# Kernel optimization log

Hardware: AMD Instinct MI355X
Metric: run time of the kernel (lower is better)

The kernel has to match this reference:

```python
import jax, jax.numpy as jnp
import numpy as np

N = 50000
IN_DIM = 256
HID = 64
HEADS = 4
OUT_DIM = 40
E = 800000
NEG_SLOPE = 0.2


def setup_inputs() -> dict:
    key = jax.random.key(0)
    ks = jax.random.split(key, 12)
    x = jax.random.normal(ks[0], (N, IN_DIM), dtype=jnp.float32)
    edge_index = jax.random.randint(ks[1], (2, E), 0, N, dtype=jnp.int64)
    s = 0.05
    W1 = jax.random.normal(ks[2], (IN_DIM, HEADS * HID), dtype=jnp.float32) * s
    att_src1 = jax.random.normal(ks[3], (HEADS, HID), dtype=jnp.float32) * s
    att_dst1 = jax.random.normal(ks[4], (HEADS, HID), dtype=jnp.float32) * s
    b1 = jnp.zeros((HEADS * HID,), dtype=jnp.float32)
    W2 = jax.random.normal(ks[5], (HEADS * HID, OUT_DIM), dtype=jnp.float32) * s
    att_src2 = jax.random.normal(ks[6], (1, OUT_DIM), dtype=jnp.float32) * s
    att_dst2 = jax.random.normal(ks[7], (1, OUT_DIM), dtype=jnp.float32) * s
    b2 = jnp.zeros((OUT_DIM,), dtype=jnp.float32)
    return {"x": x, "edge_index": edge_index, "W1": W1, "att_src1": att_src1,
            "att_dst1": att_dst1, "b1": b1, "W2": W2, "att_src2": att_src2,
            "att_dst2": att_dst2, "b2": b2}


def _gat_conv(x, src, dst, W, a_src, a_dst, b, heads, out_ch, concat):
    n = x.shape[0]
    h = (x @ W).reshape(n, heads, out_ch)              # [N,H,C]
    alpha_s = jnp.einsum('nhc,hc->nh', h, a_src)       # [N,H]
    alpha_d = jnp.einsum('nhc,hc->nh', h, a_dst)
    e = jax.nn.leaky_relu(alpha_s[src] + alpha_d[dst], NEG_SLOPE)  # [E,H]
    # segment softmax over destination neighborhoods
    m = jax.ops.segment_max(e, dst, num_segments=n)    # [N,H]
    ex = jnp.exp(e - m[dst])
    denom = jax.ops.segment_sum(ex, dst, num_segments=n)
    alpha = ex / (denom[dst] + 1e-16)                  # [E,H]
    out = jax.ops.segment_sum(h[src] * alpha[:, :, None], dst, num_segments=n)  # [N,H,C]
    out = out.reshape(n, heads * out_ch) if concat else out.mean(axis=1)
    return out + b


def reference(x, edge_index, W1, att_src1, att_dst1, b1, W2, att_src2, att_dst2, b2):
    # PyG GATConv adds self-loops by default
    loops = jnp.arange(N, dtype=edge_index.dtype)
    src = jnp.concatenate([edge_index[0], loops])
    dst = jnp.concatenate([edge_index[1], loops])
    h = _gat_conv(x, src, dst, W1, att_src1, att_dst1, b1, HEADS, HID, True)
    h = jax.nn.elu(h)
    h = _gat_conv(h, src, dst, W2, att_src2, att_dst2, b2, 1, OUT_DIM, False)
    return jax.nn.log_softmax(h, axis=1)
```

## Files before the change

### kernel.cpp

```cpp
#include <hip/hip_runtime.h>
#include <hip/hip_bf16.h>
#include <math.h>

#define NNODES 50000
#define M_PAD  50048
#define IN_DIM 256
#define HID 64
#define HEADS 4
#define OUT_DIM 40
#define NEDGES 800000
#define ETOT (NEDGES + NNODES)
#define NEG_SLOPE 0.2f
#define MAXDEG 64

typedef __attribute__((ext_vector_type(8))) short bf16x8;
typedef __attribute__((ext_vector_type(4))) float f32x4;
typedef __attribute__((ext_vector_type(2))) float f32x2;

__device__ __forceinline__ ushort f2bf(float f) {
    uint u = __float_as_uint(f);
    u += 0x7FFF + ((u >> 16) & 1);
    return (ushort)(u >> 16);
}
__device__ __forceinline__ uint fkey(float f) {
    uint u = __float_as_uint(f);
    return (u & 0x80000000u) ? ~u : (u | 0x80000000u);
}
__device__ __forceinline__ float fdec(uint k) {
    return (k & 0x80000000u) ? __uint_as_float(k & 0x7fffffffu) : __uint_as_float(~k);
}
__device__ __forceinline__ float wave_reduce_max(float v) {
    #pragma unroll
    for (int off = 32; off > 0; off >>= 1) v = fmaxf(v, __shfl_xor(v, off));
    return v;
}
__device__ __forceinline__ float wave_reduce_sum(float v) {
    #pragma unroll
    for (int off = 32; off > 0; off >>= 1) v += __shfl_xor(v, off);
    return v;
}

__device__ __forceinline__ void accum8p(f32x2* acc2, uint4 hv, float wgt) {
    f32x2 wv = {wgt, wgt};
    f32x2 v;
    v.x = __uint_as_float(hv.x << 16); v.y = __uint_as_float(hv.x & 0xFFFF0000u);
    acc2[0] += v * wv;
    v.x = __uint_as_float(hv.y << 16); v.y = __uint_as_float(hv.y & 0xFFFF0000u);
    acc2[1] += v * wv;
    v.x = __uint_as_float(hv.z << 16); v.y = __uint_as_float(hv.z & 0xFFFF0000u);
    acc2[2] += v * wv;
    v.x = __uint_as_float(hv.w << 16); v.y = __uint_as_float(hv.w & 0xFFFF0000u);
    acc2[3] += v * wv;
}
__device__ __forceinline__ float lrw(float e, float mm) {
    return __expf(fmaxf(e, NEG_SLOPE * e) - mm);
}

__global__ __launch_bounds__(256) void cvt_weights_kernel(const float* __restrict__ W1,
                                                          const float* __restrict__ W2,
                                                          ushort* __restrict__ W1t,
                                                          ushort* __restrict__ W2tb) {
    int b = blockIdx.x, t = threadIdx.x;
    if (b < 256) {
        W1t[b * 256 + t] = f2bf(W1[t * 256 + b]);
    } else {
        int idx = (b - 256) * 256 + t;
        if (idx < 48 * 264) {
            int n = idx / 264, k = idx % 264;
            W2tb[idx] = (n < OUT_DIM && k < 256) ? f2bf(W2[k * OUT_DIM + n]) : (ushort)0;
        }
    }
}

__global__ void scatter_kernel(const int* __restrict__ ei,
                               int* __restrict__ counts, int* __restrict__ col) {
    int idx = blockIdx.x * blockDim.x + threadIdx.x;
    if (idx >= ETOT) return;
    int s, d;
    if (idx < NEDGES) { s = ei[idx]; d = ei[NEDGES + idx]; }
    else { s = idx - NEDGES; d = s; }
    int pos = atomicAdd(&counts[d], 1);
    if (pos < MAXDEG) col[d * MAXDEG + pos] = s;
}

__global__ __launch_bounds__(256) void gemm1_fused(const float* __restrict__ x,
                                                   const ushort* __restrict__ W1t,
                                                   const float* __restrict__ asrc,
                                                   const float* __restrict__ adst,
                                                   ushort* __restrict__ h1b,
                                                   float* __restrict__ as1,
                                                   float* __restrict__ ad1,
                                                   uint* __restrict__ gb) {
    __shared__ ushort As[64 * 32];
    __shared__ ushort Bs[256 * 32];
    __shared__ uint smax[4];
    int t = threadIdx.x;
    int l = t & 63, wn = t >> 6;
    int m0 = blockIdx.x * 64;
    int lrow = l & 15, lks = l >> 4;
    int ks = lks ^ ((lrow >> 1) & 3);

    f32x4 acc[4][4];
    #pragma unroll
    for (int i = 0; i < 4; i++)
        #pragma unroll
        for (int j = 0; j < 4; j++) acc[i][j] = (f32x4){0.f, 0.f, 0.f, 0.f};

    for (int k0 = 0; k0 < 256; k0 += 32) {
        #pragma unroll
        for (int i = 0; i < 2; i++) {
            int idx = t + 256 * i;
            int row = idx >> 3, c4 = idx & 7;
            int grow = m0 + row;
            float4 v = make_float4(0.f, 0.f, 0.f, 0.f);
            if (grow < NNODES) v = *reinterpret_cast<const float4*>(x + (size_t)grow * 256 + k0 + c4 * 4);
            uint2 p;
            p.x = (uint)f2bf(v.x) | ((uint)f2bf(v.y) << 16);
            p.y = (uint)f2bf(v.z) | ((uint)f2bf(v.w) << 16);
            int slot = (c4 >> 1) ^ ((row >> 1) & 3);
            *reinterpret_cast<uint2*>(&As[row * 32 + slot * 8 + (c4 & 1) * 4]) = p;
        }
        #pragma unroll
        for (int i = 0; i < 4; i++) {
            int idx = t + 256 * i;
            int row = idx >> 2, skb = idx & 3;
            uint4 bv = *reinterpret_cast<const uint4*>(W1t + (size_t)row * 256 + k0 + skb * 8);
            int slot = skb ^ ((row >> 1) & 3);
            *reinterpret_cast<uint4*>(&Bs[row * 32 + slot * 8]) = bv;
        }
        __syncthreads();
        bf16x8 a_frag[4], b_frag[4];
        #pragma unroll
        for (int mf = 0; mf < 4; mf++)
            a_frag[mf] = *reinterpret_cast<const bf16x8*>(&As[(mf * 16 + lrow) * 32 + ks * 8]);
        #pragma unroll
        for (int nf = 0; nf < 4; nf++)
            b_frag[nf] = *reinterpret_cast<const bf16x8*>(&Bs[(wn * 64 + nf * 16 + lrow) * 32 + ks * 8]);
        #pragma unroll
        for (int mf = 0; mf < 4; mf++)
            #pragma unroll
            for (int nf = 0; nf < 4; nf++)
                acc[mf][nf] = __builtin_amdgcn_mfma_f32_16x16x32_bf16(a_frag[mf], b_frag[nf], acc[mf][nf], 0, 0, 0);
        __syncthreads();
    }

    #pragma unroll
    for (int mf = 0; mf < 4; mf++)
        #pragma unroll
        for (int nf = 0; nf < 4; nf++) {
            int col = wn * 64 + nf * 16 + lrow;
            #pragma unroll
            for (int r = 0; r < 4; r++) {
                int row = m0 + mf * 16 + lks * 4 + r;
                h1b[(size_t)row * 256 + col] = f2bf(acc[mf][nf][r]);
            }
        }

    float a_s[4], a_d[4];
    #pragma unroll
    for (int nf = 0; nf < 4; nf++) {
        a_s[nf] = asrc[wn * 64 + nf * 16 + lrow];
        a_d[nf] = adst[wn * 64 + nf * 16 + lrow];
    }
    float ps[4][4], pd[4][4];
    #pragma unroll
    for (int mf = 0; mf < 4; mf++)
        #pragma unroll
        for (int r = 0; r < 4; r++) {
            float s = 0.f, d = 0.f;
            #pragma unroll
            for (int nf = 0; nf < 4; nf++) {
                s += acc[mf][nf][r] * a_s[nf];
                d += acc[mf][nf][r] * a_d[nf];
            }
            ps[mf][r] = s; pd[mf][r] = d;
        }
    #pragma unroll
    for (int off = 1; off < 16; off <<= 1)
        #pragma unroll
        for (int mf = 0; mf < 4; mf++)
            #pragma unroll
            for (int r = 0; r < 4; r++) {
                ps[mf][r] += __shfl_xor(ps[mf][r], off);
                pd[mf][r] += __shfl_xor(pd[mf][r], off);
            }
    if (lrow == 0) {
        #pragma unroll
        for (int mf = 0; mf < 4; mf++)
            #pragma unroll
            for (int r = 0; r < 4; r++) {
                int row = m0 + mf * 16 + lks * 4 + r;
                if (row < NNODES) {
                    as1[row * 4 + wn] = ps[mf][r];
                    ad1[row * 4 + wn] = pd[mf][r];
                }
            }
    }
    float vmax = -INFINITY;
    #pragma unroll
    for (int mf = 0; mf < 4; mf++)
        #pragma unroll
        for (int r = 0; r < 4; r++) {
            int row = m0 + mf * 16 + lks * 4 + r;
            if (row < NNODES) vmax = fmaxf(vmax, ps[mf][r]);
        }
    vmax = fmaxf(vmax, __shfl_xor(vmax, 16));
    vmax = fmaxf(vmax, __shfl_xor(vmax, 32));
    if (l == 0) smax[wn] = fkey(vmax);
    __syncthreads();
    if (t < 4) atomicMax(&gb[t], smax[t]);
}

__device__ __forceinline__ void agg1_chunk(const int* __restrict__ p, int base, int deg,
                                           const float* __restrict__ as1,
                                           const ushort* __restrict__ h1b,
                                           int myh, uint jo, float adn, float mm,
                                           f32x2* acc2, float& ls) {
    int4 ca = *reinterpret_cast<const int4*>(p);
    int4 cb = *reinterpret_cast<const int4*>(p + 4);
    int s0 = (base + 0 < deg) ? ca.x : 0;
    int s1 = (base + 1 < deg) ? ca.y : 0;
    int s2 = (base + 2 < deg) ? ca.z : 0;
    int s3 = (base + 3 < deg) ? ca.w : 0;
    int s4 = (base + 4 < deg) ? cb.x : 0;
    int s5 = (base + 5 < deg) ? cb.y : 0;
    int s6 = (base + 6 < deg) ? cb.z : 0;
    int s7 = (base + 7 < deg) ? cb.w : 0;
    float q0 = as1[(uint)(s0 * 4 + myh)];
    float q1 = as1[(uint)(s1 * 4 + myh)];
    float q2 = as1[(uint)(s2 * 4 + myh)];
    float q3 = as1[(uint)(s3 * 4 + myh)];
    float q4 = as1[(uint)(s4 * 4 + myh)];
    float q5 = as1[(uint)(s5 * 4 + myh)];
    float q6 = as1[(uint)(s6 * 4 + myh)];
    float q7 = as1[(uint)(s7 * 4 + myh)];
    uint4 h0 = *reinterpret_cast<const uint4*>(h1b + (((uint)s0 << 8) + jo));
    uint4 h1v = *reinterpret_cast<const uint4*>(h1b + (((uint)s1 << 8) + jo));
    uint4 h2v = *reinterpret_cast<const uint4*>(h1b + (((uint)s2 << 8) + jo));
    uint4 h3v = *reinterpret_cast<const uint4*>(h1b + (((uint)s3 << 8) + jo));
    uint4 h4v = *reinterpret_cast<const uint4*>(h1b + (((uint)s4 << 8) + jo));
    uint4 h5v = *reinterpret_cast<const uint4*>(h1b + (((uint)s5 << 8) + jo));
    uint4 h6v = *reinterpret_cast<const uint4*>(h1b + (((uint)s6 << 8) + jo));
    uint4 h7v = *reinterpret_cast<const uint4*>(h1b + (((uint)s7 << 8) + jo));
    float w0 = (base + 0 < deg) ? lrw(q0 + adn, mm) : 0.f;
    float w1 = (base + 1 < deg) ? lrw(q1 + adn, mm) : 0.f;
    float w2 = (base + 2 < deg) ? lrw(q2 + adn, mm) : 0.f;
    float w3 = (base + 3 < deg) ? lrw(q3 + adn, mm) : 0.f;
    float w4 = (base + 4 < deg) ? lrw(q4 + adn, mm) : 0.f;
    float w5 = (base + 5 < deg) ? lrw(q5 + adn, mm) : 0.f;
    float w6 = (base + 6 < deg) ? lrw(q6 + adn, mm) : 0.f;
    float w7 = (base + 7 < deg) ? lrw(q7 + adn, mm) : 0.f;
    ls += ((w0 + w1) + (w2 + w3)) + ((w4 + w5) + (w6 + w7));
    accum8p(acc2, h0, w0); accum8p(acc2, h1v, w1);
    accum8p(acc2, h2v, w2); accum8p(acc2, h3v, w3);
    accum8p(acc2, h4v, w4); accum8p(acc2, h5v, w5);
    accum8p(acc2, h6v, w6); accum8p(acc2, h7v, w7);
}

__global__ __launch_bounds__(256) void agg1_kernel(const ushort* __restrict__ h1b,
                                                   const float* __restrict__ as1,
                                                   const float* __restrict__ ad1,
                                                   const int* __restrict__ cnt,
                                                   const int* __restrict__ col,
                                                   const float* __restrict__ b1,
                                                   const uint* __restrict__ gb,
                                                   ushort* __restrict__ out1b) {
    int tid = threadIdx.x;
    int lane = tid & 63, wid = tid >> 6;
    int n = blockIdx.x * 4 + wid;
    int j = lane & 31, half = lane >> 5;
    int myh = j >> 3;
    int deg = min(cnt[n], MAXDEG);
    const int* cp = col + n * MAXDEG;

    float adn = ad1[n * 4 + myh];
    float g = fdec(gb[myh]);
    float mt = g + adn;
    float mm = fmaxf(mt, NEG_SLOPE * mt);

    f32x2 acc2[4];
    #pragma unroll
    for (int k = 0; k < 4; k++) acc2[k] = (f32x2){0.f, 0.f};
    float ls = 0.f;
    uint jo = (uint)(j * 8);

    for (int done = 0; done < deg; done += 16) {
        int base = done + half * 8;
        agg1_chunk(cp + base, base, deg, as1, h1b, myh, jo, adn, mm, acc2, ls);
    }
    #pragma unroll
    for (int k = 0; k < 4; k++) {
        acc2[k].x += __shfl_xor(acc2[k].x, 32);
        acc2[k].y += __shfl_xor(acc2[k].y, 32);
    }
    ls += __shfl_xor(ls, 32);

    if (lane < 32) {
        float dinv = 1.f / (ls + 1e-16f);
        float4 bA = *reinterpret_cast<const float4*>(b1 + j * 8);
        float4 bB = *reinterpret_cast<const float4*>(b1 + j * 8 + 4);
        float o[8];
        o[0] = acc2[0].x * dinv + bA.x; o[1] = acc2[0].y * dinv + bA.y;
        o[2] = acc2[1].x * dinv + bA.z; o[3] = acc2[1].y * dinv + bA.w;
        o[4] = acc2[2].x * dinv + bB.x; o[5] = acc2[2].y * dinv + bB.y;
        o[6] = acc2[3].x * dinv + bB.z; o[7] = acc2[3].y * dinv + bB.w;
        uint4 pk;
        #pragma unroll
        for (int e8 = 0; e8 < 8; e8++) o[e8] = o[e8] > 0.f ? o[e8] : expm1f(o[e8]);
        pk.x = (uint)f2bf(o[0]) | ((uint)f2bf(o[1]) << 16);
        pk.y = (uint)f2bf(o[2]) | ((uint)f2bf(o[3]) << 16);
        pk.z = (uint)f2bf(o[4]) | ((uint)f2bf(o[5]) << 16);
        pk.w = (uint)f2bf(o[6]) | ((uint)f2bf(o[7]) << 16);
        *reinterpret_cast<uint4*>(out1b + ((uint)n * 256 + jo)) = pk;
    }
}

__global__ __launch_bounds__(256) void gemm2_fused(const ushort* __restrict__ Ag,
                                                   const ushort* __restrict__ Bg,
                                                   const float* __restrict__ a2s,
                                                   const float* __restrict__ a2d,
                                                   ushort* __restrict__ h2b,
                                                   float* __restrict__ as2,
                                                   float* __restrict__ ad2,
                                                   uint* __restrict__ gb) {
    __shared__ ushort Bs[48 * 264];
    __shared__ uint smax;
    int t = threadIdx.x;
    int l = t & 63, w = t >> 6;
    int lrow = l & 15, lks = l >> 4;
    if (t == 0) smax = 0u;
    for (int idx = t; idx < 48 * 264 / 8; idx += 256)
        reinterpret_cast<uint4*>(Bs)[idx] = reinterpret_cast<const uint4*>(Bg)[idx];
    __syncthreads();

    int m0 = blockIdx.x * 64 + w * 16;
    f32x4 acc[3];
    #pragma unroll
    for (int nf = 0; nf < 3; nf++) acc[nf] = (f32x4){0.f, 0.f, 0.f, 0.f};

    #pragma unroll
    for (int k0 = 0; k0 < 256; k0 += 32) {
        bf16x8 af = *reinterpret_cast<const bf16x8*>(Ag + (size_t)(m0 + lrow) * 256 + k0 + lks * 8);
        #pragma unroll
        for (int nf = 0; nf < 3; nf++) {
            bf16x8 bf = *reinterpret_cast<const bf16x8*>(&Bs[(nf * 16 + lrow) * 264 + k0 + lks * 8]);
            acc[nf] = __builtin_amdgcn_mfma_f32_16x16x32_bf16(af, bf, acc[nf], 0, 0, 0);
        }
    }

    float a_s[3], a_d[3];
    #pragma unroll
    for (int nf = 0; nf < 3; nf++) {
        int c = nf * 16 + lrow;
        a_s[nf] = (c < OUT_DIM) ? a2s[c] : 0.f;
        a_d[nf] = (c < OUT_DIM) ? a2d[c] : 0.f;
    }
    float ps[4], pd[4];
    #pragma unroll
    for (int r = 0; r < 4; r++) {
        float s = 0.f, d = 0.f;
        #pragma unroll
        for (int nf = 0; nf < 3; nf++) { s += acc[nf][r] * a_s[nf]; d += acc[nf][r] * a_d[nf]; }
        ps[r] = s; pd[r] = d;
    }
    #pragma unroll
    for (int nf = 0; nf < 3; nf++) {
        int c = nf * 16 + lrow;
        if (c < OUT_DIM) {
            #pragma unroll
            for (int r = 0; r < 4; r++) {
                int row = m0 + lks * 4 + r;
                if (row < NNODES) h2b[(size_t)row * OUT_DIM + c] = f2bf(acc[nf][r]);
            }
        }
    }
    #pragma unroll
    for (int off = 1; off < 16; off <<= 1)
        #pragma unroll
        for (int r = 0; r < 4; r++) {
            ps[r] += __shfl_xor(ps[r], off);
            pd[r] += __shfl_xor(pd[r], off);
        }
    if (lrow == 0) {
        #pragma unroll
        for (int r = 0; r < 4; r++) {
            int row = m0 + lks * 4 + r;
            if (row < NNODES) { as2[row] = ps[r]; ad2[row] = pd[r]; }
        }
    }
    float vmax = -INFINITY;
    #pragma unroll
    for (int r = 0; r < 4; r++) {
        int row = m0 + lks * 4 + r;
        if (row < NNODES) vmax = fmaxf(vmax, ps[r]);
    }
    vmax = fmaxf(vmax, __shfl_xor(vmax, 16));
    vmax = fmaxf(vmax, __shfl_xor(vmax, 32));
    if (l == 0) atomicMax(&smax, fkey(vmax));
    __syncthreads();
    if (t == 0) atomicMax(&gb[4], smax);
}

__device__ __forceinline__ void agg2_chunk(const int* __restrict__ p, int base, int deg,
                                           const float* __restrict__ as2,
                                           const ushort* __restrict__ h2b,
                                           bool act, uint jo, float adn, float mm,
                                           f32x2& a2, float& ls) {
    int4 ca = *reinterpret_cast<const int4*>(p);
    int4 cb = *reinterpret_cast<const int4*>(p + 4);
    int s0 = (base + 0 < deg) ? ca.x : 0;
    int s1 = (base + 1 < deg) ? ca.y : 0;
    int s2 = (base + 2 < deg) ? ca.z : 0;
    int s3 = (base + 3 < deg) ? ca.w : 0;
    int s4 = (base + 4 < deg) ? cb.x : 0;
    int s5 = (base + 5 < deg) ? cb.y : 0;
    int s6 = (base + 6 < deg) ? cb.z : 0;
    int s7 = (base + 7 < deg) ? cb.w : 0;
    float q0 = as2[(uint)s0], q1 = as2[(uint)s1], q2 = as2[(uint)s2], q3 = as2[(uint)s3];
    float q4 = as2[(uint)s4], q5 = as2[(uint)s5], q6 = as2[(uint)s6], q7 = as2[(uint)s7];
    uint v0 = 0, v1 = 0, v2 = 0, v3 = 0, v4 = 0, v5 = 0, v6 = 0, v7 = 0;
    if (act) {
        v0 = *reinterpret_cast<const uint*>(h2b + ((uint)s0 * 40 + jo));
        v1 = *reinterpret_cast<const uint*>(h2b + ((uint)s1 * 40 + jo));
        v2 = *reinterpret_cast<const uint*>(h2b + ((uint)s2 * 40 + jo));
        v3 = *reinterpret_cast<const uint*>(h2b + ((uint)s3 * 40 + jo));
        v4 = *reinterpret_cast<const uint*>(h2b + ((uint)s4 * 40 + jo));
        v5 = *reinterpret_cast<const uint*>(h2b + ((uint)s5 * 40 + jo));
        v6 = *reinterpret_cast<const uint*>(h2b + ((uint)s6 * 40 + jo));
        v7 = *reinterpret_cast<const uint*>(h2b + ((uint)s7 * 40 + jo));
    }
    float w0 = (base + 0 < deg) ? lrw(q0 + adn, mm) : 0.f;
    float w1 = (base + 1 < deg) ? lrw(q1 + adn, mm) : 0.f;
    float w2 = (base + 2 < deg) ? lrw(q2 + adn, mm) : 0.f;
    float w3 = (base + 3 < deg) ? lrw(q3 + adn, mm) : 0.f;
    float w4 = (base + 4 < deg) ? lrw(q4 + adn, mm) : 0.f;
    float w5 = (base + 5 < deg) ? lrw(q5 + adn, mm) : 0.f;
    float w6 = (base + 6 < deg) ? lrw(q6 + adn, mm) : 0.f;
    float w7 = (base + 7 < deg) ? lrw(q7 + adn, mm) : 0.f;
    ls += ((w0 + w1) + (w2 + w3)) + ((w4 + w5) + (w6 + w7));
    f32x2 hv;
    hv.x = __uint_as_float(v0 << 16); hv.y = __uint_as_float(v0 & 0xFFFF0000u);
    a2 += hv * (f32x2){w0, w0};
    hv.x = __uint_as_float(v1 << 16); hv.y = __uint_as_float(v1 & 0xFFFF0000u);
    a2 += hv * (f32x2){w1, w1};
    hv.x = __uint_as_float(v2 << 16); hv.y = __uint_as_float(v2 & 0xFFFF0000u);
    a2 += hv * (f32x2){w2, w2};
    hv.x = __uint_as_float(v3 << 16); hv.y = __uint_as_float(v3 & 0xFFFF0000u);
    a2 += hv * (f32x2){w3, w3};
    hv.x = __uint_as_float(v4 << 16); hv.y = __uint_as_float(v4 & 0xFFFF0000u);
    a2 += hv * (f32x2){w4, w4};
    hv.x = __uint_as_float(v5 << 16); hv.y = __uint_as_float(v5 & 0xFFFF0000u);
    a2 += hv * (f32x2){w5, w5};
    hv.x = __uint_as_float(v6 << 16); hv.y = __uint_as_float(v6 & 0xFFFF0000u);
    a2 += hv * (f32x2){w6, w6};
    hv.x = __uint_as_float(v7 << 16); hv.y = __uint_as_float(v7 & 0xFFFF0000u);
    a2 += hv * (f32x2){w7, w7};
}

__global__ __launch_bounds__(256) void agg2_kernel(const ushort* __restrict__ h2b,
                                                   const float* __restrict__ as2,
                                                   const float* __restrict__ ad2,
                                                   const int* __restrict__ cnt,
                                                   const int* __restrict__ col,
                                                   const float* __restrict__ b2,
                                                   const uint* __restrict__ gb,
                                                   float* __restrict__ out) {
    int tid = threadIdx.x;
    int lane = tid & 63, wid = tid >> 6;
    int n = blockIdx.x * 4 + wid;
    int j = lane & 31, half = lane >> 5;
    int deg = min(cnt[n], MAXDEG);
    const int* cp = col + n * MAXDEG;
    float adn = ad2[n];
    float g = fdec(gb[4]);
    float mt = g + adn;
    float mm = fmaxf(mt, NEG_SLOPE * mt);

    bool act = j < 20;
    uint jo = (uint)(j * 2);
    f32x2 a2 = {0.f, 0.f};
    float ls = 0.f;

    for (int done = 0; done < deg; done += 16) {
        int base = done + half * 8;
        agg2_chunk(cp + base, base, deg, as2, h2b, act, jo, adn, mm, a2, ls);
    }
    a2.x += __shfl_xor(a2.x, 32);
    a2.y += __shfl_xor(a2.y, 32);
    ls += __shfl_xor(ls, 32);

    bool lead = lane < 20;
    float v0 = -INFINITY, v1 = -INFINITY;
    if (lead) {
        float2 bb = *reinterpret_cast<const float2*>(b2 + 2 * j);
        float dinv = 1.f / (ls + 1e-16f);
        v0 = a2.x * dinv + bb.x;
        v1 = a2.y * dinv + bb.y;
    }
    float mx = wave_reduce_max(fmaxf(v0, v1));
    float es = lead ? (__expf(v0 - mx) + __expf(v1 - mx)) : 0.f;
    float ssum = wave_reduce_sum(es);
    float lg = logf(ssum);
    if (lead) {
        float2 o2 = make_float2(v0 - mx - lg, v1 - mx - lg);
        *reinterpret_cast<float2*>(out + (size_t)n * OUT_DIM + 2 * j) = o2;
    }
}

extern "C" void kernel_launch(void* const* d_in, const int* in_sizes, int n_in,
                              void* d_out, int out_size, void* d_ws, size_t ws_size,
                              hipStream_t stream) {
    const float* x        = (const float*)d_in[0];
    const int*   ei       = (const int*)d_in[1];
    const float* W1       = (const float*)d_in[2];
    const float* att_src1 = (const float*)d_in[3];
    const float* att_dst1 = (const float*)d_in[4];
    const float* b1       = (const float*)d_in[5];
    const float* W2       = (const float*)d_in[6];
    const float* att_src2 = (const float*)d_in[7];
    const float* att_dst2 = (const float*)d_in[8];
    const float* b2       = (const float*)d_in[9];
    float* out = (float*)d_out;

    char* ws = (char*)d_ws;
    auto alloc = [&](size_t bytes) {
        char* p = ws;
        ws += (bytes + 255) & ~(size_t)255;
        return p;
    };
    ushort* h1b    = (ushort*)alloc((size_t)M_PAD * 256 * 2);
    ushort* out1b  = (ushort*)alloc((size_t)M_PAD * 256 * 2);
    ushort* W1t    = (ushort*)alloc((size_t)256 * 256 * 2);
    ushort* W2tb   = (ushort*)alloc((size_t)48 * 264 * 2);
    ushort* h2b    = (ushort*)alloc((size_t)NNODES * OUT_DIM * 2);
    float*  as1    = (float*)alloc((size_t)NNODES * 4 * 4);
    float*  ad1    = (float*)alloc((size_t)NNODES * 4 * 4);
    float*  as2    = (float*)alloc((size_t)NNODES * 4);
    float*  ad2    = (float*)alloc((size_t)NNODES * 4);
    int*    counts = (int*)alloc((size_t)(NNODES + 8) * 4);
    uint*   gmaxb  = (uint*)(counts + NNODES);
    int*    col    = (int*)alloc((size_t)NNODES * MAXDEG * 4);
    if ((size_t)(ws - (char*)d_ws) > ws_size) return;

    hipMemsetAsync(counts, 0, (size_t)(NNODES + 8) * 4, stream);

    cvt_weights_kernel<<<256 + (48 * 264 + 255) / 256, 256, 0, stream>>>(W1, W2, W1t, W2tb);

    int eb = (ETOT + 255) / 256;
    scatter_kernel<<<eb, 256, 0, stream>>>(ei, counts, col);

    gemm1_fused<<<M_PAD / 64, 256, 0, stream>>>(x, W1t, att_src1, att_dst1,
                                                h1b, as1, ad1, gmaxb);
    agg1_kernel<<<NNODES / 4, 256, 0, stream>>>(h1b, as1, ad1, counts, col, b1, gmaxb, out1b);

    gemm2_fused<<<M_PAD / 64, 256, 0, stream>>>(out1b, W2tb, att_src2, att_dst2,
                                                h2b, as2, ad2, gmaxb);
    agg2_kernel<<<NNODES / 4, 256, 0, stream>>>(h2b, as2, ad2, counts, col, b2, gmaxb, out);
}
```

Measured before the change: 213.3 us.

## Fold layer-2 attention projections into agg1 and merge prep kernels

```diff
diff --git a/kernel.cpp b/kernel.cpp
--- a/kernel.cpp
+++ b/kernel.cpp
@@ -39,7 +39,6 @@
     for (int off = 32; off > 0; off >>= 1) v += __shfl_xor(v, off);
     return v;
 }
-
 __device__ __forceinline__ void accum8p(f32x2* acc2, uint4 hv, float wgt) {
     f32x2 wv = {wgt, wgt};
     f32x2 v;
@@ -56,31 +55,41 @@
     return __expf(fmaxf(e, NEG_SLOPE * e) - mm);
 }
 
-__global__ __launch_bounds__(256) void cvt_weights_kernel(const float* __restrict__ W1,
-                                                          const float* __restrict__ W2,
-                                                          ushort* __restrict__ W1t,
-                                                          ushort* __restrict__ W2tb) {
+__global__ void prep_kernel(const float* __restrict__ W1, const float* __restrict__ W2,
+                            const float* __restrict__ a2s, const float* __restrict__ a2d,
+                            const int* __restrict__ ei,
+                            ushort* __restrict__ W1t, ushort* __restrict__ W2tb,
+                            float* __restrict__ wa_s, float* __restrict__ wa_d,
+                            int* __restrict__ counts, int* __restrict__ col) {
     int b = blockIdx.x, t = threadIdx.x;
     if (b < 256) {
         W1t[b * 256 + t] = f2bf(W1[t * 256 + b]);
-    } else {
+    } else if (b < 306) {
         int idx = (b - 256) * 256 + t;
         if (idx < 48 * 264) {
             int n = idx / 264, k = idx % 264;
             W2tb[idx] = (n < OUT_DIM && k < 256) ? f2bf(W2[k * OUT_DIM + n]) : (ushort)0;
         }
-    }
-}
-
-__global__ void scatter_kernel(const int* __restrict__ ei,
-                               int* __restrict__ counts, int* __restrict__ col) {
-    int idx = blockIdx.x * blockDim.x + threadIdx.x;
-    if (idx >= ETOT) return;
-    int s, d;
-    if (idx < NEDGES) { s = ei[idx]; d = ei[NEDGES + idx]; }
-    else { s = idx - NEDGES; d = s; }
-    int pos = atomicAdd(&counts[d], 1);
-    if (pos < MAXDEG) col[d * MAXDEG + pos] = s;
+    } else if (b == 306) {
+        float ss = 0.f, sd = 0.f;
+        #pragma unroll 8
+        for (int c = 0; c < OUT_DIM; c++) {
+            float wv = W2[t * OUT_DIM + c];
+            ss += wv * a2s[c];
+            sd += wv * a2d[c];
+        }
+        wa_s[t] = ss;
+        wa_d[t] = sd;
+    } else {
+        int idx = (b - 307) * 256 + t;
+        if (idx < ETOT) {
+            int s, d;
+            if (idx < NEDGES) { s = ei[idx]; d = ei[NEDGES + idx]; }
+            else { s = idx - NEDGES; d = s; }
+            int pos = atomicAdd(&counts[d], 1);
+            if (pos < MAXDEG) col[d * MAXDEG + pos] = s;
+        }
+    }
 }
 
 __global__ __launch_bounds__(256) void gemm1_fused(const float* __restrict__ x,
@@ -264,7 +273,11 @@
                                                    const int* __restrict__ col,
                                                    const float* __restrict__ b1,
                                                    const uint* __restrict__ gb,
-                                                   ushort* __restrict__ out1b) {
+                                                   const float* __restrict__ wa_s,
+                                                   const float* __restrict__ wa_d,
+                                                   ushort* __restrict__ out1b,
+                                                   float* __restrict__ as2,
+                                                   float* __restrict__ ad2) {
     int tid = threadIdx.x;
     int lane = tid & 63, wid = tid >> 6;
     int n = blockIdx.x * 4 + wid;
@@ -295,18 +308,32 @@
     }
     ls += __shfl_xor(ls, 32);
 
+    float dinv = 1.f / (ls + 1e-16f);
+    float4 bA = *reinterpret_cast<const float4*>(b1 + j * 8);
+    float4 bB = *reinterpret_cast<const float4*>(b1 + j * 8 + 4);
+    float4 wsA = *reinterpret_cast<const float4*>(wa_s + j * 8);
+    float4 wsB = *reinterpret_cast<const float4*>(wa_s + j * 8 + 4);
+    float4 wdA = *reinterpret_cast<const float4*>(wa_d + j * 8);
+    float4 wdB = *reinterpret_cast<const float4*>(wa_d + j * 8 + 4);
+    float o[8];
+    o[0] = acc2[0].x * dinv + bA.x; o[1] = acc2[0].y * dinv + bA.y;
+    o[2] = acc2[1].x * dinv + bA.z; o[3] = acc2[1].y * dinv + bA.w;
+    o[4] = acc2[2].x * dinv + bB.x; o[5] = acc2[2].y * dinv + bB.y;
+    o[6] = acc2[3].x * dinv + bB.z; o[7] = acc2[3].y * dinv + bB.w;
+    #pragma unroll
+    for (int e8 = 0; e8 < 8; e8++) o[e8] = o[e8] > 0.f ? o[e8] : expm1f(o[e8]);
+    float dps = o[0] * wsA.x + o[1] * wsA.y + o[2] * wsA.z + o[3] * wsA.w
+              + o[4] * wsB.x + o[5] * wsB.y + o[6] * wsB.z + o[7] * wsB.w;
+    float dpd = o[0] * wdA.x + o[1] * wdA.y + o[2] * wdA.z + o[3] * wdA.w
+              + o[4] * wdB.x + o[5] * wdB.y + o[6] * wdB.z + o[7] * wdB.w;
+    #pragma unroll
+    for (int off = 1; off < 32; off <<= 1) {
+        dps += __shfl_xor(dps, off);
+        dpd += __shfl_xor(dpd, off);
+    }
+    if (lane == 0) { as2[n] = dps; ad2[n] = dpd; }
     if (lane < 32) {
-        float dinv = 1.f / (ls + 1e-16f);
-        float4 bA = *reinterpret_cast<const float4*>(b1 + j * 8);
-        float4 bB = *reinterpret_cast<const float4*>(b1 + j * 8 + 4);
-        float o[8];
-        o[0] = acc2[0].x * dinv + bA.x; o[1] = acc2[0].y * dinv + bA.y;
-        o[2] = acc2[1].x * dinv + bA.z; o[3] = acc2[1].y * dinv + bA.w;
-        o[4] = acc2[2].x * dinv + bB.x; o[5] = acc2[2].y * dinv + bB.y;
-        o[6] = acc2[3].x * dinv + bB.z; o[7] = acc2[3].y * dinv + bB.w;
         uint4 pk;
-        #pragma unroll
-        for (int e8 = 0; e8 < 8; e8++) o[e8] = o[e8] > 0.f ? o[e8] : expm1f(o[e8]);
         pk.x = (uint)f2bf(o[0]) | ((uint)f2bf(o[1]) << 16);
         pk.y = (uint)f2bf(o[2]) | ((uint)f2bf(o[3]) << 16);
         pk.z = (uint)f2bf(o[4]) | ((uint)f2bf(o[5]) << 16);
@@ -315,20 +342,15 @@
     }
 }
 
-__global__ __launch_bounds__(256) void gemm2_fused(const ushort* __restrict__ Ag,
-                                                   const ushort* __restrict__ Bg,
-                                                   const float* __restrict__ a2s,
-                                                   const float* __restrict__ a2d,
-                                                   ushort* __restrict__ h2b,
-                                                   float* __restrict__ as2,
-                                                   float* __restrict__ ad2,
-                                                   uint* __restrict__ gb) {
+__global__ __launch_bounds__(256) void gemm2_kernel(const ushort* __restrict__ Ag,
+                                                    const ushort* __restrict__ Bg,
+                                                    const float* __restrict__ as2,
+                                                    ushort* __restrict__ h2b,
+                                                    uint* __restrict__ gb) {
     __shared__ ushort Bs[48 * 264];
-    __shared__ uint smax;
     int t = threadIdx.x;
     int l = t & 63, w = t >> 6;
     int lrow = l & 15, lks = l >> 4;
-    if (t == 0) smax = 0u;
     for (int idx = t; idx < 48 * 264 / 8; idx += 256)
         reinterpret_cast<uint4*>(Bs)[idx] = reinterpret_cast<const uint4*>(Bg)[idx];
     __syncthreads();
@@ -346,22 +368,6 @@
             bf16x8 bf = *reinterpret_cast<const bf16x8*>(&Bs[(nf * 16 + lrow) * 264 + k0 + lks * 8]);
             acc[nf] = __builtin_amdgcn_mfma_f32_16x16x32_bf16(af, bf, acc[nf], 0, 0, 0);
         }
-    }
-
-    float a_s[3], a_d[3];
-    #pragma unroll
-    for (int nf = 0; nf < 3; nf++) {
-        int c = nf * 16 + lrow;
-        a_s[nf] = (c < OUT_DIM) ? a2s[c] : 0.f;
-        a_d[nf] = (c < OUT_DIM) ? a2d[c] : 0.f;
-    }
-    float ps[4], pd[4];
-    #pragma unroll
-    for (int r = 0; r < 4; r++) {
-        float s = 0.f, d = 0.f;
-        #pragma unroll
-        for (int nf = 0; nf < 3; nf++) { s += acc[nf][r] * a_s[nf]; d += acc[nf][r] * a_d[nf]; }
-        ps[r] = s; pd[r] = d;
     }
     #pragma unroll
     for (int nf = 0; nf < 3; nf++) {
@@ -374,31 +380,12 @@
             }
         }
     }
-    #pragma unroll
-    for (int off = 1; off < 16; off <<= 1)
-        #pragma unroll
-        for (int r = 0; r < 4; r++) {
-            ps[r] += __shfl_xor(ps[r], off);
-            pd[r] += __shfl_xor(pd[r], off);
-        }
-    if (lrow == 0) {
-        #pragma unroll
-        for (int r = 0; r < 4; r++) {
-            int row = m0 + lks * 4 + r;
-            if (row < NNODES) { as2[row] = ps[r]; ad2[row] = pd[r]; }
-        }
-    }
-    float vmax = -INFINITY;
-    #pragma unroll
-    for (int r = 0; r < 4; r++) {
-        int row = m0 + lks * 4 + r;
-        if (row < NNODES) vmax = fmaxf(vmax, ps[r]);
-    }
-    vmax = fmaxf(vmax, __shfl_xor(vmax, 16));
-    vmax = fmaxf(vmax, __shfl_xor(vmax, 32));
-    if (l == 0) atomicMax(&smax, fkey(vmax));
-    __syncthreads();
-    if (t == 0) atomicMax(&gb[4], smax);
+    if (t < 64) {
+        int row = blockIdx.x * 64 + t;
+        float v = (row < NNODES) ? as2[row] : -INFINITY;
+        v = wave_reduce_max(v);
+        if (t == 0) atomicMax(&gb[4], fkey(v));
+    }
 }
 
 __device__ __forceinline__ void agg2_chunk(const int* __restrict__ p, int base, int deg,
@@ -537,6 +524,8 @@
     float*  ad1    = (float*)alloc((size_t)NNODES * 4 * 4);
     float*  as2    = (float*)alloc((size_t)NNODES * 4);
     float*  ad2    = (float*)alloc((size_t)NNODES * 4);
+    float*  wa_s   = (float*)alloc((size_t)256 * 4);
+    float*  wa_d   = (float*)alloc((size_t)256 * 4);
     int*    counts = (int*)alloc((size_t)(NNODES + 8) * 4);
     uint*   gmaxb  = (uint*)(counts + NNODES);
     int*    col    = (int*)alloc((size_t)NNODES * MAXDEG * 4);
@@ -544,16 +533,14 @@
 
     hipMemsetAsync(counts, 0, (size_t)(NNODES + 8) * 4, stream);
 
-    cvt_weights_kernel<<<256 + (48 * 264 + 255) / 256, 256, 0, stream>>>(W1, W2, W1t, W2tb);
-
-    int eb = (ETOT + 255) / 256;
-    scatter_kernel<<<eb, 256, 0, stream>>>(ei, counts, col);
+    int prep_blocks = 307 + (ETOT + 255) / 256;
+    prep_kernel<<<prep_blocks, 256, 0, stream>>>(W1, W2, att_src2, att_dst2, ei,
+                                                 W1t, W2tb, wa_s, wa_d, counts, col);
 
     gemm1_fused<<<M_PAD / 64, 256, 0, stream>>>(x, W1t, att_src1, att_dst1,
                                                 h1b, as1, ad1, gmaxb);
-    agg1_kernel<<<NNODES / 4, 256, 0, stream>>>(h1b, as1, ad1, counts, col, b1, gmaxb, out1b);
-
-    gemm2_fused<<<M_PAD / 64, 256, 0, stream>>>(out1b, W2tb, att_src2, att_dst2,
-                                                h2b, as2, ad2, gmaxb);
+    agg1_kernel<<<NNODES / 4, 256, 0, stream>>>(h1b, as1, ad1, counts, col, b1, gmaxb,
+                                                wa_s, wa_d, out1b, as2, ad2);
+    gemm2_kernel<<<M_PAD / 64, 256, 0, stream>>>(out1b, W2tb, as2, h2b, gmaxb);
     agg2_kernel<<<NNODES / 4, 256, 0, stream>>>(h2b, as2, ad2, counts, col, b2, gmaxb, out);
 }
```

Result: no change. 209.6 us (-1.7%).
